# Optimization experiments

Hardware: AMD Instinct MI355X
Metric: run time of the kernel (lower is better)

The kernel has to match this reference:

```python
import jax, jax.numpy as jnp
import numpy as np

EPS = 1e-4
B, D, DOUT = 8192, 4096, 4096


def setup_inputs() -> dict:
    key = jax.random.key(0)
    k1, k2, k3 = jax.random.split(key, 3)
    x = jax.random.normal(k1, (B, D), dtype=jnp.float32)
    # Linear layer params (torch nn.Linear: y = x @ W.T + b)
    W = jax.random.normal(k2, (DOUT, D), dtype=jnp.float32) * (1.0 / np.sqrt(D))
    b = jax.random.normal(k3, (DOUT,), dtype=jnp.float32) * 0.01
    return {"x": x, "W": W, "b": b}


def reference(x, W, b):
    # hess = sum_b x[b] outer x[b] + eps*I  == X^T X + eps*I (a GEMM, not a
    # materialized [B,D,D] broadcast like the torch source)
    d = x.shape[1]
    hess = jnp.einsum('bi,bj->ij', x, x) + EPS * jnp.eye(d, dtype=x.dtype)
    out = x @ W.T + b  # wrapped nn.Linear
    return out, hess
```

## Files before the change

### kernel.cpp

```cpp
#include <hip/hip_runtime.h>
#include <hip/hip_bf16.h>

#define BDIM 8192
#define DDIM 4096
#define DOUTD 4096

typedef __attribute__((ext_vector_type(8))) short short8;
typedef __attribute__((ext_vector_type(16))) float floatx16;

__device__ inline unsigned short f32_to_bf16_rne(float f) {
    unsigned int u = __float_as_uint(f);
    unsigned int lsb = (u >> 16) & 1u;
    u += 0x7fffu + lsb;
    return (unsigned short)(u >> 16);
}

__device__ inline void gload_lds16(const void* g, void* lds) {
    __builtin_amdgcn_global_load_lds(
        (const __attribute__((address_space(1))) void*)g,
        (__attribute__((address_space(3))) void*)lds,
        16, 0, 0);
}

__global__ __launch_bounds__(256)
void convert_transpose_x(const float* __restrict__ x,
                         unsigned short* __restrict__ xb,
                         unsigned short* __restrict__ xT) {
    __shared__ __align__(16) unsigned short tile[64][72];
    const int t = threadIdx.x;
    const int tb = blockIdx.x * 64;
    const int td = blockIdx.y * 64;
#pragma unroll
    for (int p = 0; p < 4; ++p) {
        int c = t + p * 256;
        int row  = c >> 4;
        int col4 = (c & 15) << 2;
        float4 v = *(const float4*)&x[(size_t)(tb + row) * DDIM + td + col4];
        ushort4 o;
        o.x = f32_to_bf16_rne(v.x);
        o.y = f32_to_bf16_rne(v.y);
        o.z = f32_to_bf16_rne(v.z);
        o.w = f32_to_bf16_rne(v.w);
        *(ushort4*)&xb[(size_t)(tb + row) * DDIM + td + col4] = o;
        tile[col4 + 0][row] = o.x;
        tile[col4 + 1][row] = o.y;
        tile[col4 + 2][row] = o.z;
        tile[col4 + 3][row] = o.w;
    }
    __syncthreads();
#pragma unroll
    for (int p = 0; p < 4; ++p) {
        int c = t + p * 256;
        int drow = c >> 4;
        int b4   = (c & 15) << 2;
        ushort4 o = *(const ushort4*)&tile[drow][b4];
        *(ushort4*)&xT[(size_t)(td + drow) * BDIM + tb + b4] = o;
    }
}

__global__ __launch_bounds__(256)
void convert_w_kernel(const float* __restrict__ W, unsigned short* __restrict__ Wb) {
    size_t i = ((size_t)blockIdx.x * 256 + threadIdx.x) * 4;
    float4 v = *(const float4*)&W[i];
    ushort4 o;
    o.x = f32_to_bf16_rne(v.x);
    o.y = f32_to_bf16_rne(v.y);
    o.z = f32_to_bf16_rne(v.z);
    o.w = f32_to_bf16_rne(v.w);
    *(ushort4*)&Wb[i] = o;
}

template <bool HESS>
__global__ __launch_bounds__(256)
void gemm_nt(const unsigned short* __restrict__ A,
             const unsigned short* __restrict__ B,
             const float* __restrict__ bias,
             float* __restrict__ C,
             int M, int N, int K) {
    constexpr int BK = 32;
    __shared__ __align__(16) unsigned short As[128 * BK];
    __shared__ __align__(16) unsigned short Bs[128 * BK];

    const int t    = threadIdx.x;
    const int lane = t & 63;
    const int wave = t >> 6;
    const int hi   = lane >> 5;
    const int lm   = lane & 31;
    const int h    = (lane >> 2) & 3;
    const size_t bm = (size_t)blockIdx.x * 128;
    const size_t bn = (size_t)blockIdx.y * 128;
    const int wm = (wave & 1) * 64;
    const int wn = (wave >> 1) * 64;

    const int srow = t >> 2;
    const int kcg  = ((t & 3) ^ ((t >> 4) & 3)) * 8;
    const unsigned short* gA0 = A + (bm + srow) * (size_t)K + kcg;
    const unsigned short* gA1 = gA0 + (size_t)64 * K;
    const unsigned short* gB0 = B + (bn + srow) * (size_t)K + kcg;
    const unsigned short* gB1 = gB0 + (size_t)64 * K;
    char* ldsA0 = (char*)As + wave * 1024;
    char* ldsA1 = ldsA0 + 4096;
    char* ldsB0 = (char*)Bs + wave * 1024;
    char* ldsB1 = ldsB0 + 4096;

    floatx16 acc[2][2];
#pragma unroll
    for (int i = 0; i < 2; ++i)
#pragma unroll
        for (int j = 0; j < 2; ++j)
#pragma unroll
            for (int g = 0; g < 16; ++g)
                acc[i][j][g] = 0.f;

    int aoff[2][2], boff[2][2];
#pragma unroll
    for (int i = 0; i < 2; ++i)
#pragma unroll
        for (int s = 0; s < 2; ++s) {
            int pos = ((2 * s + hi) ^ h) * 8;
            aoff[i][s] = (wm + 32 * i + lm) * BK + pos;
            boff[i][s] = (wn + 32 * i + lm) * BK + pos;
        }

    for (int k0 = 0; k0 < K; k0 += BK) {
        gload_lds16(gA0 + k0, ldsA0);
        gload_lds16(gA1 + k0, ldsA1);
        gload_lds16(gB0 + k0, ldsB0);
        gload_lds16(gB1 + k0, ldsB1);
        __syncthreads();

        short8 af[2][2], bf[2][2];
#pragma unroll
        for (int s = 0; s < 2; ++s)
#pragma unroll
            for (int i = 0; i < 2; ++i) {
                af[i][s] = *(const short8*)&As[aoff[i][s]];
                bf[i][s] = *(const short8*)&Bs[boff[i][s]];
            }
#pragma unroll
        for (int s = 0; s < 2; ++s) {
            acc[0][0] = __builtin_amdgcn_mfma_f32_32x32x16_bf16(af[0][s], bf[0][s], acc[0][0], 0, 0, 0);
            acc[0][1] = __builtin_amdgcn_mfma_f32_32x32x16_bf16(af[0][s], bf[1][s], acc[0][1], 0, 0, 0);
            acc[1][0] = __builtin_amdgcn_mfma_f32_32x32x16_bf16(af[1][s], bf[0][s], acc[1][0], 0, 0, 0);
            acc[1][1] = __builtin_amdgcn_mfma_f32_32x32x16_bf16(af[1][s], bf[1][s], acc[1][1], 0, 0, 0);
        }
        __syncthreads();
    }

    float bv[2];
#pragma unroll
    for (int j = 0; j < 2; ++j)
        bv[j] = HESS ? 0.f : bias[bn + wn + j * 32 + lm];
#pragma unroll
    for (int i = 0; i < 2; ++i) {
        const size_t mbase = bm + wm + i * 32 + 4 * hi;
#pragma unroll
        for (int j = 0; j < 2; ++j) {
            const size_t n = bn + wn + j * 32 + lm;
#pragma unroll
            for (int reg = 0; reg < 16; ++reg) {
                const size_t m = mbase + (reg & 3) + 8 * (reg >> 2);
                float v = acc[i][j][reg] + bv[j];
                if (HESS && m == n) v += 1e-4f;
                C[m * N + n] = v;
            }
        }
    }
}

extern "C" void kernel_launch(void* const* d_in, const int* in_sizes, int n_in,
                              void* d_out, int out_size, void* d_ws, size_t ws_size,
                              hipStream_t stream) {
    const float* x = (const float*)d_in[0];
    const float* W = (const float*)d_in[1];
    const float* b = (const float*)d_in[2];

    float* out  = (float*)d_out;
    float* hess = out + (size_t)BDIM * DOUTD;

    unsigned short* xb = (unsigned short*)d_ws;
    unsigned short* xT = xb + (size_t)BDIM * DDIM;
    unsigned short* Wb = xT + (size_t)BDIM * DDIM;

    convert_transpose_x<<<dim3(BDIM / 64, DDIM / 64), 256, 0, stream>>>(x, xb, xT);
    convert_w_kernel<<<((size_t)DOUTD * DDIM) / 1024, 256, 0, stream>>>(W, Wb);

    gemm_nt<false><<<dim3(BDIM / 128, DOUTD / 128), 256, 0, stream>>>(
        xb, Wb, b, out, BDIM, DOUTD, DDIM);
    gemm_nt<true><<<dim3(DDIM / 128, DDIM / 128), 256, 0, stream>>>(
        xT, xT, nullptr, hess, DDIM, DDIM, BDIM);
}
```

Measured before the change: 1.004 ms.

## Rewrite GEMM as 256x256 tile, 8-wave kernel with double-buffered LDS pipeline

Replaces the 128x128, BK=32, 4-wave GEMM with a 256x256, BK=64, 8-wave kernel. Global-to-LDS loads for the next k-tiles are issued in quarters interleaved with MFMA phases, with explicit vmcnt/lgkmcnt waits, raw barriers and s_setprio around the MFMA bursts. This targets the fully serialized load-sync-compute loop and the low operand reuse of small tiles in both GEMMs. The cost is 128KB of LDS per block, which limits occupancy, plus fragile hand-placed waits and barriers that must stay consistent with the issue order.

Result: faster. 892.9 us (-11.1%).

```diff
diff --git a/kernel.cpp b/kernel.cpp
--- a/kernel.cpp
+++ b/kernel.cpp
@@ -70,97 +70,172 @@
     *(ushort4*)&Wb[i] = o;
 }
 
+#define CFENCE() asm volatile("" ::: "memory")
+#define BAR() do { CFENCE(); __builtin_amdgcn_s_barrier(); CFENCE(); } while (0)
+#define MFMA_BF16 __builtin_amdgcn_mfma_f32_32x32x16_bf16
+
 template <bool HESS>
-__global__ __launch_bounds__(256)
-void gemm_nt(const unsigned short* __restrict__ A,
+__global__ __launch_bounds__(512, 2)
+void gemm256(const unsigned short* __restrict__ A,
              const unsigned short* __restrict__ B,
              const float* __restrict__ bias,
              float* __restrict__ C,
              int M, int N, int K) {
-    constexpr int BK = 32;
-    __shared__ __align__(16) unsigned short As[128 * BK];
-    __shared__ __align__(16) unsigned short Bs[128 * BK];
+    __shared__ __align__(16) unsigned short As[32768];
+    __shared__ __align__(16) unsigned short Bs[32768];
 
     const int t    = threadIdx.x;
     const int lane = t & 63;
-    const int wave = t >> 6;
+    const int w    = t >> 6;
+    const int lm   = lane & 31;
     const int hi   = lane >> 5;
-    const int lm   = lane & 31;
-    const int h    = (lane >> 2) & 3;
-    const size_t bm = (size_t)blockIdx.x * 128;
-    const size_t bn = (size_t)blockIdx.y * 128;
-    const int wm = (wave & 1) * 64;
-    const int wn = (wave >> 1) * 64;
-
-    const int srow = t >> 2;
-    const int kcg  = ((t & 3) ^ ((t >> 4) & 3)) * 8;
-    const unsigned short* gA0 = A + (bm + srow) * (size_t)K + kcg;
-    const unsigned short* gA1 = gA0 + (size_t)64 * K;
-    const unsigned short* gB0 = B + (bn + srow) * (size_t)K + kcg;
-    const unsigned short* gB1 = gB0 + (size_t)64 * K;
-    char* ldsA0 = (char*)As + wave * 1024;
-    char* ldsA1 = ldsA0 + 4096;
-    char* ldsB0 = (char*)Bs + wave * 1024;
-    char* ldsB1 = ldsB0 + 4096;
-
-    floatx16 acc[2][2];
-#pragma unroll
-    for (int i = 0; i < 2; ++i)
+    const int key  = lm >> 2;
+    const int wm   = w >> 2;
+    const int wn   = w & 3;
+    const size_t bm = (size_t)blockIdx.y * 256;
+    const size_t bn = (size_t)blockIdx.x * 256;
+    const int NT = K >> 6;
+
+    const int r8  = lane >> 3;
+    const int c8  = lane & 7;
+    const int rl0 = w * 16 + r8;
+    const int rl1 = rl0 + 8;
+    const int kc0 = c8 ^ ((w * 4 + (lane >> 5)) & 7);
+    const int kc1 = c8 ^ ((w * 4 + 2 + (lane >> 5)) & 7);
+    const unsigned short* gA0 = A + (bm + rl0) * (size_t)K + kc0 * 8;
+    const unsigned short* gA1 = A + (bm + rl1) * (size_t)K + kc1 * 8;
+    const unsigned short* gB0 = B + (bn + rl0) * (size_t)K + kc0 * 8;
+    const unsigned short* gB1 = B + (bn + rl1) * (size_t)K + kc1 * 8;
+    char* ldsA = (char*)As + w * 2048;
+    char* ldsB = (char*)Bs + w * 2048;
+    const size_t halfK = (size_t)128 * K;
+
+#define STAGE_A(tj, h, buf) do {                                   \
+        const size_t _ko = (size_t)(tj) * 64 + (size_t)(h) * halfK;\
+        char* _d = ldsA + (buf) * 32768 + (h) * 16384;             \
+        gload_lds16(gA0 + _ko, _d);                                \
+        gload_lds16(gA1 + _ko, _d + 1024);                         \
+    } while (0)
+#define STAGE_B(tj, h, buf) do {                                   \
+        const size_t _ko = (size_t)(tj) * 64 + (size_t)(h) * halfK;\
+        char* _d = ldsB + (buf) * 32768 + (h) * 16384;             \
+        gload_lds16(gB0 + _ko, _d);                                \
+        gload_lds16(gB1 + _ko, _d + 1024);                         \
+    } while (0)
+
+    const int AROW = (wm * 128 + lm) * 64;
+    const int BROW = (wn * 32 + lm) * 64;
+    int swz[4];
+#pragma unroll
+    for (int s = 0; s < 4; ++s) swz[s] = (((2 * s + hi) ^ key) << 3);
+
+    floatx16 acc[4][2];
+#pragma unroll
+    for (int i = 0; i < 4; ++i)
 #pragma unroll
         for (int j = 0; j < 2; ++j)
 #pragma unroll
             for (int g = 0; g < 16; ++g)
                 acc[i][j][g] = 0.f;
 
-    int aoff[2][2], boff[2][2];
-#pragma unroll
-    for (int i = 0; i < 2; ++i)
-#pragma unroll
-        for (int s = 0; s < 2; ++s) {
-            int pos = ((2 * s + hi) ^ h) * 8;
-            aoff[i][s] = (wm + 32 * i + lm) * BK + pos;
-            boff[i][s] = (wn + 32 * i + lm) * BK + pos;
-        }
-
-    for (int k0 = 0; k0 < K; k0 += BK) {
-        gload_lds16(gA0 + k0, ldsA0);
-        gload_lds16(gA1 + k0, ldsA1);
-        gload_lds16(gB0 + k0, ldsB0);
-        gload_lds16(gB1 + k0, ldsB1);
-        __syncthreads();
-
-        short8 af[2][2], bf[2][2];
-#pragma unroll
-        for (int s = 0; s < 2; ++s)
-#pragma unroll
-            for (int i = 0; i < 2; ++i) {
-                af[i][s] = *(const short8*)&As[aoff[i][s]];
-                bf[i][s] = *(const short8*)&Bs[boff[i][s]];
-            }
-#pragma unroll
-        for (int s = 0; s < 2; ++s) {
-            acc[0][0] = __builtin_amdgcn_mfma_f32_32x32x16_bf16(af[0][s], bf[0][s], acc[0][0], 0, 0, 0);
-            acc[0][1] = __builtin_amdgcn_mfma_f32_32x32x16_bf16(af[0][s], bf[1][s], acc[0][1], 0, 0, 0);
-            acc[1][0] = __builtin_amdgcn_mfma_f32_32x32x16_bf16(af[1][s], bf[0][s], acc[1][0], 0, 0, 0);
-            acc[1][1] = __builtin_amdgcn_mfma_f32_32x32x16_bf16(af[1][s], bf[1][s], acc[1][1], 0, 0, 0);
-        }
-        __syncthreads();
-    }
+    short8 af0[2][4], af1[2][4], bf[4];
+
+    STAGE_B(0, 0, 0);
+    STAGE_A(0, 0, 0);
+    STAGE_A(0, 1, 0);
+    STAGE_B(0, 1, 0);
+    STAGE_B(1, 0, 1);
+    STAGE_A(1, 0, 1);
+    STAGE_A(1, 1, 1);
+    asm volatile("s_waitcnt vmcnt(6)" ::: "memory");
+    BAR();
+
+    for (int j = 0; j < NT; ++j) {
+        const int cur = j & 1;
+        const int ab  = cur * 16384;
+
+#pragma unroll
+        for (int mi = 0; mi < 2; ++mi)
+#pragma unroll
+            for (int s = 0; s < 4; ++s)
+                af0[mi][s] = *(const short8*)&As[ab + AROW + mi * 2048 + swz[s]];
+#pragma unroll
+        for (int s = 0; s < 4; ++s)
+            bf[s] = *(const short8*)&Bs[ab + BROW + swz[s]];
+        if (j + 1 < NT) STAGE_B(j + 1, 1, cur ^ 1);
+        BAR();
+        __builtin_amdgcn_s_setprio(1);
+#pragma unroll
+        for (int s = 0; s < 4; ++s) {
+            acc[0][0] = MFMA_BF16(af0[0][s], bf[s], acc[0][0], 0, 0, 0);
+            acc[1][0] = MFMA_BF16(af0[1][s], bf[s], acc[1][0], 0, 0, 0);
+        }
+        __builtin_amdgcn_s_setprio(0);
+        asm volatile("s_waitcnt lgkmcnt(0)" ::: "memory");
+        BAR();
+
+#pragma unroll
+        for (int mi = 0; mi < 2; ++mi)
+#pragma unroll
+            for (int s = 0; s < 4; ++s)
+                af1[mi][s] = *(const short8*)&As[ab + AROW + 4096 + mi * 2048 + swz[s]];
+        if (j + 2 < NT) STAGE_B(j + 2, 0, cur);
+        BAR();
+        __builtin_amdgcn_s_setprio(1);
+#pragma unroll
+        for (int s = 0; s < 4; ++s) {
+            acc[2][0] = MFMA_BF16(af1[0][s], bf[s], acc[2][0], 0, 0, 0);
+            acc[3][0] = MFMA_BF16(af1[1][s], bf[s], acc[3][0], 0, 0, 0);
+        }
+        __builtin_amdgcn_s_setprio(0);
+        asm volatile("s_waitcnt lgkmcnt(0)" ::: "memory");
+        BAR();
+
+#pragma unroll
+        for (int s = 0; s < 4; ++s)
+            bf[s] = *(const short8*)&Bs[ab + BROW + 8192 + swz[s]];
+        if (j + 2 < NT) STAGE_A(j + 2, 0, cur);
+        BAR();
+        __builtin_amdgcn_s_setprio(1);
+#pragma unroll
+        for (int s = 0; s < 4; ++s) {
+            acc[2][1] = MFMA_BF16(af1[0][s], bf[s], acc[2][1], 0, 0, 0);
+            acc[3][1] = MFMA_BF16(af1[1][s], bf[s], acc[3][1], 0, 0, 0);
+        }
+        __builtin_amdgcn_s_setprio(0);
+        asm volatile("s_waitcnt lgkmcnt(0)" ::: "memory");
+        BAR();
+
+        if (j + 2 < NT) STAGE_A(j + 2, 1, cur);
+        BAR();
+        __builtin_amdgcn_s_setprio(1);
+#pragma unroll
+        for (int s = 0; s < 4; ++s) {
+            acc[0][1] = MFMA_BF16(af0[0][s], bf[s], acc[0][1], 0, 0, 0);
+            acc[1][1] = MFMA_BF16(af0[1][s], bf[s], acc[1][1], 0, 0, 0);
+        }
+        __builtin_amdgcn_s_setprio(0);
+        if (j < NT - 2)       asm volatile("s_waitcnt vmcnt(6)" ::: "memory");
+        else if (j == NT - 2) asm volatile("s_waitcnt vmcnt(0)" ::: "memory");
+        BAR();
+    }
+#undef STAGE_A
+#undef STAGE_B
 
     float bv[2];
 #pragma unroll
-    for (int j = 0; j < 2; ++j)
-        bv[j] = HESS ? 0.f : bias[bn + wn + j * 32 + lm];
-#pragma unroll
-    for (int i = 0; i < 2; ++i) {
-        const size_t mbase = bm + wm + i * 32 + 4 * hi;
-#pragma unroll
-        for (int j = 0; j < 2; ++j) {
-            const size_t n = bn + wn + j * 32 + lm;
+    for (int n2 = 0; n2 < 2; ++n2)
+        bv[n2] = HESS ? 0.f : bias[bn + n2 * 128 + wn * 32 + lm];
+#pragma unroll
+    for (int m4 = 0; m4 < 4; ++m4) {
+        const size_t mbase = bm + wm * 128 + (m4 >> 1) * 64 + (m4 & 1) * 32 + 4 * hi;
+#pragma unroll
+        for (int n2 = 0; n2 < 2; ++n2) {
+            const size_t n = bn + n2 * 128 + wn * 32 + lm;
 #pragma unroll
             for (int reg = 0; reg < 16; ++reg) {
                 const size_t m = mbase + (reg & 3) + 8 * (reg >> 2);
-                float v = acc[i][j][reg] + bv[j];
+                float v = acc[m4][n2][reg] + bv[n2];
                 if (HESS && m == n) v += 1e-4f;
                 C[m * N + n] = v;
             }
@@ -185,8 +260,8 @@
     convert_transpose_x<<<dim3(BDIM / 64, DDIM / 64), 256, 0, stream>>>(x, xb, xT);
     convert_w_kernel<<<((size_t)DOUTD * DDIM) / 1024, 256, 0, stream>>>(W, Wb);
 
-    gemm_nt<false><<<dim3(BDIM / 128, DOUTD / 128), 256, 0, stream>>>(
+    gemm256<false><<<dim3(DOUTD / 256, BDIM / 256), 512, 0, stream>>>(
         xb, Wb, b, out, BDIM, DOUTD, DDIM);
-    gemm_nt<true><<<dim3(DDIM / 128, DDIM / 128), 256, 0, stream>>>(
+    gemm256<true><<<dim3(DDIM / 256, DDIM / 256), 512, 0, stream>>>(
         xT, xT, nullptr, hess, DDIM, DDIM, BDIM);
 }
```
